# Kernel tuning notes

Hardware: AMD Instinct MI355X
Metric: run time of the kernel (lower is better)

The kernel has to match this reference:

```python
import jax, jax.numpy as jnp
import numpy as np

D_MODEL = 1024
NUM_HEADS = 16
D_HEAD = D_MODEL // NUM_HEADS


def setup_inputs() -> dict:
    key = jax.random.key(0)
    ks = jax.random.split(key, 8)
    B, S = 2, 2048
    query_x = jax.random.normal(ks[0], (B, S, D_MODEL), dtype=jnp.float32)
    key_x = jax.random.normal(ks[1], (B, S, D_MODEL), dtype=jnp.float32)
    value_x = jax.random.normal(ks[2], (B, S, D_MODEL), dtype=jnp.float32)
    mask = jnp.zeros((S, S), dtype=jnp.float32)  # additive mask, broadcast over B,H
    scale = np.sqrt(2.0 / D_MODEL)  # kaiming-ish init
    w_query = jax.random.normal(ks[3], (D_MODEL, D_MODEL), dtype=jnp.float32) * scale
    w_key = jax.random.normal(ks[4], (D_MODEL, D_MODEL), dtype=jnp.float32) * scale
    w_value = jax.random.normal(ks[5], (D_MODEL, D_MODEL), dtype=jnp.float32) * scale
    w0 = jax.random.normal(ks[6], (D_MODEL, D_MODEL), dtype=jnp.float32) * scale
    return {"query_x": query_x, "key_x": key_x, "value_x": value_x, "mask": mask,
            "w_query": w_query, "w_key": w_key, "w_value": w_value, "w0": w0}


def reference(query_x, key_x, value_x, mask, w_query, w_key, w_value, w0):
    B, S, _ = query_x.shape
    # nn.Linear applies x @ W.T; weights stored [out, in]
    def proj(x, w):
        y = jnp.einsum('bsd,ed->bse', x, w)              # [B,S,D]
        return y.reshape(B, S, NUM_HEADS, D_HEAD).transpose(0, 2, 1, 3)  # [B,H,S,Dh]
    q = proj(query_x, w_query)
    k = proj(key_x, w_key)
    v = proj(value_x, w_value)
    scores = jnp.einsum('bhqd,bhkd->bhqk', q, k) / jnp.sqrt(jnp.float32(D_HEAD))
    scores = scores + mask  # broadcast additive mask
    attn = jax.nn.softmax(scores, axis=-1)
    out = jnp.einsum('bhqk,bhkd->bhqd', attn, v)         # [B,H,S,Dh]
    out = out.transpose(0, 2, 1, 3).reshape(B, S, NUM_HEADS * D_HEAD)
    return jnp.einsum('bsd,ed->bse', out, w0)
```

## Files before the change

### kernel.cpp

```cpp
#include <hip/hip_runtime.h>
#include <hip/hip_bf16.h>
#include <stdint.h>

#define D_MODEL 1024
#define NH 16
#define DH 64
#define SEQ 2048
#define MROWS 4096
#define LOG2E 1.44269504088896340736f

typedef unsigned short ushort_t;
typedef __attribute__((ext_vector_type(4))) float f32x4;
typedef __attribute__((ext_vector_type(16))) float f32x16;
typedef __attribute__((ext_vector_type(4))) unsigned short us4;
typedef __attribute__((ext_vector_type(8))) unsigned short us8;
typedef __attribute__((ext_vector_type(4))) unsigned int u32x4;
typedef __attribute__((ext_vector_type(8))) __bf16 bf16x8;

__device__ __forceinline__ f32x4 mfma16(us8 a, us8 b, f32x4 c) {
    return __builtin_amdgcn_mfma_f32_16x16x32_bf16(
        __builtin_bit_cast(bf16x8, a), __builtin_bit_cast(bf16x8, b), c, 0, 0, 0);
}
__device__ __forceinline__ f32x16 mfma32(us8 a, us8 b, f32x16 c) {
    return __builtin_amdgcn_mfma_f32_32x32x16_bf16(
        __builtin_bit_cast(bf16x8, a), __builtin_bit_cast(bf16x8, b), c, 0, 0, 0);
}

__device__ __forceinline__ unsigned int cvtpk(float lo, float hi) {
    unsigned int r;
    asm("v_cvt_pk_bf16_f32 %0, %1, %2" : "=v"(r) : "v"(lo), "v"(hi));
    return r;
}
__device__ __forceinline__ ushort_t f2bf1(float f) {
    return (ushort_t)(cvtpk(f, f) & 0xffffu);
}

__device__ __forceinline__ float exp2_fast(float x) {
#if __has_builtin(__builtin_amdgcn_exp2f)
    return __builtin_amdgcn_exp2f(x);
#else
    float r; asm("v_exp_f32 %0, %1" : "=v"(r) : "v"(x)); return r;
#endif
}

__device__ __forceinline__ void gload16(const void* g, void* l) {
    __builtin_amdgcn_global_load_lds(
        (const __attribute__((address_space(1))) void*)g,
        (__attribute__((address_space(3))) void*)l, 16, 0, 0);
}

__global__ __launch_bounds__(256) void conv_multi(
    const float* __restrict__ s0, ushort_t* __restrict__ d0,
    const float* __restrict__ s1, ushort_t* __restrict__ d1,
    const float* __restrict__ s2, ushort_t* __restrict__ d2,
    const float* __restrict__ s3, ushort_t* __restrict__ d3, int n4)
{
    int z = blockIdx.z;
    const float* s = z == 0 ? s0 : z == 1 ? s1 : z == 2 ? s2 : s3;
    ushort_t* d    = z == 0 ? d0 : z == 1 ? d1 : z == 2 ? d2 : d3;
    int i = blockIdx.x * 256 + threadIdx.x;
    int stride = gridDim.x * 256;
    for (; i < n4; i += stride) {
        float4 v = ((const float4*)s)[i];
        uint2 pr;
        pr.x = cvtpk(v.x, v.y);
        pr.y = cvtpk(v.z, v.w);
        ((uint2*)d)[i] = pr;
    }
}

__global__ __launch_bounds__(256) void mask_flags(const float* __restrict__ mask,
                                                  int* __restrict__ flags)
{
    int qt = blockIdx.x, kt = blockIdx.y;
    int t = threadIdx.x;
    bool nz = false;
#pragma unroll
    for (int i = 0; i < 4; i++) {
        int idx = t + i * 256;
        int row = idx >> 4, c4 = (idx & 15) * 4;
        float4 v = *(const float4*)(mask + (size_t)(qt * 64 + row) * SEQ + kt * 64 + c4);
        nz |= (v.x != 0.f) | (v.y != 0.f) | (v.z != 0.f) | (v.w != 0.f);
    }
    if (__any((int)nz) && (t & 63) == 0) atomicOr(&flags[qt * 32 + kt], 1);
}

__device__ __forceinline__ void gemm_stage(const ushort_t* __restrict__ A,
                                           const ushort_t* __restrict__ B,
                                           int m0, int n0, int t, int w, int k0,
                                           ushort_t* sA, ushort_t* sB)
{
#pragma unroll
    for (int r = 0; r < 4; r++) {
        int chunk = r * 256 + t;
        int row = chunk >> 3, c8 = (chunk & 7) * 8;
        gload16(A + (size_t)(m0 + row) * D_MODEL + k0 + c8,
                &sA[(r * 256 + w * 64) * 8]);
    }
#pragma unroll
    for (int r = 0; r < 2; r++) {
        int chunk = r * 256 + t;
        int row = chunk >> 3, c8 = (chunk & 7) * 8;
        gload16(B + (size_t)(n0 + row) * D_MODEL + k0 + c8,
                &sB[(r * 256 + w * 64) * 8]);
    }
}

__device__ __forceinline__ void gemm_core(const ushort_t* __restrict__ A,
                                          const ushort_t* __restrict__ B,
                                          int m0, int n0, int t,
                                          ushort_t* sA, ushort_t* sB,
                                          f32x4 acc[4][2])
{
    const int lane = t & 63, w = t >> 6;
    const int lr = lane & 15, lg = lane >> 4;
    const int wm = (w >> 1) * 64, wn = (w & 1) * 32;

    gemm_stage(A, B, m0, n0, t, w, 0, sA, sB);
    __syncthreads();

    for (int it = 0; it < D_MODEL / 64; ++it) {
        const int cur = it & 1;
        const ushort_t* cA = sA + cur * (128 * 64);
        const ushort_t* cB = sB + cur * (64 * 64);

        us8 af[4][2], bfr[2][2];
#pragma unroll
        for (int i = 0; i < 4; i++)
#pragma unroll
            for (int ks = 0; ks < 2; ks++)
                af[i][ks] = *(const us8*)&cA[(wm + i * 16 + lr) * 64 + ks * 32 + 8 * lg];
#pragma unroll
        for (int j = 0; j < 2; j++)
#pragma unroll
            for (int ks = 0; ks < 2; ks++)
                bfr[j][ks] = *(const us8*)&cB[(wn + j * 16 + lr) * 64 + ks * 32 + 8 * lg];

        if (it + 1 < D_MODEL / 64)
            gemm_stage(A, B, m0, n0, t, w, (it + 1) * 64,
                       sA + (cur ^ 1) * (128 * 64), sB + (cur ^ 1) * (64 * 64));

#pragma unroll
        for (int i = 0; i < 4; i++)
#pragma unroll
            for (int j = 0; j < 2; j++)
#pragma unroll
                for (int ks = 0; ks < 2; ks++)
                    acc[i][j] = mfma16(af[i][ks], bfr[j][ks], acc[i][j]);

        __syncthreads();
    }
}

__global__ __launch_bounds__(256) void gemm_qk(const ushort_t* __restrict__ A0,
                                               const ushort_t* __restrict__ A1,
                                               const ushort_t* __restrict__ Wq,
                                               const ushort_t* __restrict__ Wk,
                                               ushort_t* __restrict__ Qo,
                                               ushort_t* __restrict__ Ko)
{
    __shared__ ushort_t sA[2][128 * 64];
    __shared__ ushort_t sB[2][64 * 64];
    const int z = blockIdx.z;
    const ushort_t* A = z ? A1 : A0;
    const ushort_t* W = z ? Wk : Wq;
    ushort_t* C = z ? Ko : Qo;
    const float scale = z ? 1.0f : 0.125f * LOG2E;
    const int t = threadIdx.x, lane = t & 63, w = t >> 6;
    const int lr = lane & 15, lg = lane >> 4;
    const int wm = (w >> 1) * 64, wn = (w & 1) * 32;
    const int m0 = blockIdx.x * 128, n0 = blockIdx.y * 64;

    f32x4 acc[4][2];
    f32x4 zero = {0.f, 0.f, 0.f, 0.f};
#pragma unroll
    for (int i = 0; i < 4; i++)
#pragma unroll
        for (int j = 0; j < 2; j++) acc[i][j] = zero;
    gemm_core(A, W, m0, n0, t, &sA[0][0], &sB[0][0], acc);

#pragma unroll
    for (int i = 0; i < 4; i++)
#pragma unroll
        for (int j = 0; j < 2; j++)
#pragma unroll
            for (int r = 0; r < 4; r++) {
                int m = m0 + wm + i * 16 + 4 * lg + r;
                int n = n0 + wn + j * 16 + lr;
                int b = m >> 11, s = m & 2047;
                int h = n >> 6, dh = n & 63;
                C[(((size_t)(b * NH + h)) * SEQ + s) * DH + dh] = f2bf1(acc[i][j][r] * scale);
            }
}

__global__ __launch_bounds__(256) void gemm_v(const ushort_t* __restrict__ A,
                                              const ushort_t* __restrict__ W,
                                              ushort_t* __restrict__ VT)
{
    __shared__ ushort_t sA[2][128 * 64];
    __shared__ ushort_t sB[2][64 * 64];
    const int t = threadIdx.x, lane = t & 63, w = t >> 6;
    const int lr = lane & 15, lg = lane >> 4;
    const int wm = (w >> 1) * 64, wn = (w & 1) * 32;
    const int m0 = blockIdx.x * 128, n0 = blockIdx.y * 64;

    f32x4 acc[4][2];
    f32x4 zero = {0.f, 0.f, 0.f, 0.f};
#pragma unroll
    for (int i = 0; i < 4; i++)
#pragma unroll
        for (int j = 0; j < 2; j++) acc[i][j] = zero;
    gemm_core(A, W, m0, n0, t, &sA[0][0], &sB[0][0], acc);

#pragma unroll
    for (int i = 0; i < 4; i++)
#pragma unroll
        for (int j = 0; j < 2; j++) {
            int m = m0 + wm + i * 16 + 4 * lg;
            int n = n0 + wn + j * 16 + lr;
            int b = m >> 11, s = m & 2047;
            int h = n >> 6, dh = n & 63;
            uint2 pr;
            pr.x = cvtpk(acc[i][j][0], acc[i][j][1]);
            pr.y = cvtpk(acc[i][j][2], acc[i][j][3]);
            *(uint2*)&VT[(((size_t)(b * NH + h)) * DH + dh) * SEQ + s] = pr;
        }
}

__global__ __launch_bounds__(256) void gemm_o(const ushort_t* __restrict__ A,
                                              const ushort_t* __restrict__ W,
                                              float* __restrict__ C)
{
    __shared__ ushort_t sA[2][128 * 64];
    __shared__ ushort_t sB[2][64 * 64];
    const int t = threadIdx.x, lane = t & 63, w = t >> 6;
    const int lr = lane & 15, lg = lane >> 4;
    const int wm = (w >> 1) * 64, wn = (w & 1) * 32;
    const int m0 = blockIdx.x * 128, n0 = blockIdx.y * 64;

    f32x4 acc[4][2];
    f32x4 zero = {0.f, 0.f, 0.f, 0.f};
#pragma unroll
    for (int i = 0; i < 4; i++)
#pragma unroll
        for (int j = 0; j < 2; j++) acc[i][j] = zero;
    gemm_core(A, W, m0, n0, t, &sA[0][0], &sB[0][0], acc);

#pragma unroll
    for (int i = 0; i < 4; i++)
#pragma unroll
        for (int j = 0; j < 2; j++)
#pragma unroll
            for (int r = 0; r < 4; r++) {
                int m = m0 + wm + i * 16 + 4 * lg + r;
                int n = n0 + wn + j * 16 + lr;
                C[(size_t)m * D_MODEL + n] = acc[i][j][r];
            }
}

__global__ __launch_bounds__(256, 2) void attn_fwd(const ushort_t* __restrict__ Q,
                                                   const ushort_t* __restrict__ K,
                                                   const ushort_t* __restrict__ VT,
                                                   const float* __restrict__ mask,
                                                   const int* __restrict__ flags,
                                                   ushort_t* __restrict__ O)
{
    __shared__ ushort_t sK[2][64 * 64];
    __shared__ ushort_t sVT[2][64 * 64];

    const int t = threadIdx.x, lane = t & 63, w = t >> 6;
    const int l31 = lane & 31, lh = lane >> 5;
    const int id = blockIdx.x;
    const int bh = (id & 7) * 4 + ((id >> 3) >> 4);
    const int qt = (id >> 3) & 15;
    const int b = bh >> 4, h = bh & 15;
    const int q = qt * 128 + w * 32 + l31;

    unsigned long long blt = __ballot(flags[(qt * 2 + lh) * 32 + l31] != 0);
    const unsigned int fl = (unsigned int)(blt | (blt >> 32));

    us8 qfr[4];
#pragma unroll
    for (int ks = 0; ks < 4; ks++)
        qfr[ks] = *(const us8*)(Q + ((size_t)bh * SEQ + q) * DH + ks * 16 + 8 * lh);

    f32x16 acc_o[2];
#pragma unroll
    for (int d = 0; d < 2; d++)
#pragma unroll
        for (int r = 0; r < 16; r++) acc_o[d][r] = 0.f;
    float acc_l = 0.f;

    const ushort_t* Kb = K + (size_t)bh * SEQ * DH;
    const ushort_t* Vb = VT + (size_t)bh * DH * SEQ;

    const ushort_t* kp[2];
    const ushort_t* vp[2];
#pragma unroll
    for (int r = 0; r < 2; r++) {
        int j = r * 256 + t;
        int row = j >> 3, cc = (j & 7) ^ (row & 7);
        kp[r] = Kb + (size_t)row * DH + cc * 8;
        vp[r] = Vb + (size_t)row * SEQ + cc * 8;
    }

#define STAGE(kvt_, buf_)                                                     \
    {                                                                         \
        _Pragma("unroll")                                                     \
        for (int r = 0; r < 2; r++)                                           \
            gload16(kp[r] + (size_t)(kvt_) * (64 * DH),                       \
                    &sK[buf_][(r * 256 + w * 64) * 8]);                       \
        _Pragma("unroll")                                                     \
        for (int r = 0; r < 2; r++)                                           \
            gload16(vp[r] + (size_t)(kvt_) * 64,                              \
                    &sVT[buf_][(r * 256 + w * 64) * 8]);                      \
    }

    STAGE(0, 0);
    __syncthreads();

    for (int kvt = 0; kvt < SEQ / 64; ++kvt) {
        const int cur = kvt & 1;
        const char* cK = (const char*)sK[cur];
        const char* cV = (const char*)sVT[cur];

        f32x16 sacc[2];
#pragma unroll
        for (int kb = 0; kb < 2; kb++)
#pragma unroll
            for (int r = 0; r < 16; r++) sacc[kb][r] = 0.f;
        __builtin_amdgcn_s_setprio(1);
#pragma unroll
        for (int ks = 0; ks < 4; ks++)
#pragma unroll
            for (int kb = 0; kb < 2; kb++) {
                int row = kb * 32 + l31;
                int by = (row * 128 + (ks * 16 + 8 * lh) * 2) ^ ((row & 7) << 4);
                us8 kf = *(const us8*)(cK + by);
                sacc[kb] = mfma32(kf, qfr[ks], sacc[kb]);
            }
        __builtin_amdgcn_s_setprio(0);

        us8 vf[4][2];
#pragma unroll
        for (int ks = 0; ks < 4; ks++)
#pragma unroll
            for (int dblk = 0; dblk < 2; dblk++) {
                int row = dblk * 32 + l31;
                int by = (row * 128 + (ks * 16 + 8 * lh) * 2) ^ ((row & 7) << 4);
                vf[ks][dblk] = *(const us8*)(cV + by);
            }

        if (kvt + 1 < SEQ / 64) STAGE(kvt + 1, cur ^ 1);

        if ((fl >> kvt) & 1u) {
#pragma unroll
            for (int kb = 0; kb < 2; kb++)
#pragma unroll
                for (int r = 0; r < 16; r++) {
                    int kcol = kb * 32 + (r & 3) + 8 * (r >> 2) + 4 * lh;
                    sacc[kb][r] += mask[(size_t)q * SEQ + kvt * 64 + kcol] * LOG2E;
                }
        }

        float rs = 0.f;
#pragma unroll
        for (int kb = 0; kb < 2; kb++)
#pragma unroll
            for (int r = 0; r < 16; r++) {
                float p = exp2_fast(sacc[kb][r]);
                sacc[kb][r] = p;
                rs += p;
            }
        rs += __shfl_xor(rs, 32);
        acc_l += rs;

        __builtin_amdgcn_s_setprio(1);
#pragma unroll
        for (int ks = 0; ks < 4; ks++) {
            const int kb = ks >> 1, u = ks & 1;
            unsigned int W0 = cvtpk(sacc[kb][8 * u + 0], sacc[kb][8 * u + 1]);
            unsigned int W1 = cvtpk(sacc[kb][8 * u + 2], sacc[kb][8 * u + 3]);
            unsigned int W2 = cvtpk(sacc[kb][8 * u + 4], sacc[kb][8 * u + 5]);
            unsigned int W3 = cvtpk(sacc[kb][8 * u + 6], sacc[kb][8 * u + 7]);
            asm("v_permlane32_swap_b32 %0, %1" : "+v"(W0), "+v"(W2));
            asm("v_permlane32_swap_b32 %0, %1" : "+v"(W1), "+v"(W3));
            u32x4 pw;
            pw[0] = W0; pw[1] = W1; pw[2] = W2; pw[3] = W3;
            us8 pf = __builtin_bit_cast(us8, pw);
#pragma unroll
            for (int dblk = 0; dblk < 2; dblk++)
                acc_o[dblk] = mfma32(vf[ks][dblk], pf, acc_o[dblk]);
        }
        __builtin_amdgcn_s_setprio(0);

        __syncthreads();
    }

    float inv = 1.f / acc_l;
    ushort_t* Orow = O + ((size_t)(b * SEQ) + q) * D_MODEL + h * DH;
#pragma unroll
    for (int dblk = 0; dblk < 2; dblk++)
#pragma unroll
        for (int g = 0; g < 4; g++) {
            unsigned int lo = cvtpk(acc_o[dblk][4 * g + 0] * inv,
                                    acc_o[dblk][4 * g + 1] * inv);
            unsigned int hi = cvtpk(acc_o[dblk][4 * g + 2] * inv,
                                    acc_o[dblk][4 * g + 3] * inv);
            uint2 pr; pr.x = lo; pr.y = hi;
            *(uint2*)(Orow + dblk * 32 + 8 * g + 4 * lh) = pr;
        }
#undef STAGE
}

extern "C" void kernel_launch(void* const* d_in, const int* in_sizes, int n_in,
                              void* d_out, int out_size, void* d_ws, size_t ws_size,
                              hipStream_t stream)
{
    const float* qx   = (const float*)d_in[0];
    const float* kx   = (const float*)d_in[1];
    const float* vx   = (const float*)d_in[2];
    const float* mask = (const float*)d_in[3];
    const float* wq   = (const float*)d_in[4];
    const float* wk   = (const float*)d_in[5];
    const float* wv   = (const float*)d_in[6];
    const float* w0   = (const float*)d_in[7];
    float* out = (float*)d_out;

    char* ws = (char*)d_ws;
    const size_t MB = 1024 * 1024;
    ushort_t* A0 = (ushort_t*)(ws);
    ushort_t* A1 = (ushort_t*)(ws + 8 * MB);
    ushort_t* Wq = (ushort_t*)(ws + 16 * MB);
    ushort_t* Wk = (ushort_t*)(ws + 18 * MB);
    ushort_t* Wv = (ushort_t*)(ws + 20 * MB);
    ushort_t* W0 = (ushort_t*)(ws + 22 * MB);
    ushort_t* VT = (ushort_t*)(ws + 24 * MB);
    int* flags   = (int*)(ws + 32 * MB);
    ushort_t* AO = A1;
    ushort_t* Qb = (ushort_t*)d_out;
    ushort_t* Kb = (ushort_t*)d_out + 4 * MB;

    hipMemsetAsync(flags, 0, 32 * 32 * sizeof(int), stream);
    mask_flags<<<dim3(32, 32), 256, 0, stream>>>(mask, flags);

    conv_multi<<<dim3(256, 1, 4), 256, 0, stream>>>(wq, Wq, wk, Wk, wv, Wv, w0, W0, 262144);
    conv_multi<<<dim3(1024, 1, 2), 256, 0, stream>>>(qx, A0, kx, A1, qx, A0, qx, A0, 1048576);

    gemm_qk<<<dim3(32, 16, 2), 256, 0, stream>>>(A0, A1, Wq, Wk, Qb, Kb);

    conv_multi<<<dim3(1024, 1, 1), 256, 0, stream>>>(vx, A0, vx, A0, vx, A0, vx, A0, 1048576);
    gemm_v<<<dim3(32, 16), 256, 0, stream>>>(A0, Wv, VT);

    attn_fwd<<<512, 256, 0, stream>>>(Qb, Kb, VT, mask, flags, AO);

    gemm_o<<<dim3(32, 16), 256, 0, stream>>>(AO, W0, out);
}
```

Measured before the change: 142.3 us.

## Fuse fp32-to-bf16 activation conversion into a single QKV projection GEMM

Drops the separate conversion kernels for the query, key and value activations. The projection GEMM now reads fp32 inputs directly and converts them to bf16 while staging into shared memory. The Q, K and V projections are merged into one launch over three grid slices. This removes the bf16 intermediate round-trips and several launches, but the A-tile staging becomes synchronous register loads rather than async global-to-LDS copies, and each element is re-read in fp32 once per N-tile.

```diff
diff --git a/kernel.cpp b/kernel.cpp
--- a/kernel.cpp
+++ b/kernel.cpp
@@ -85,10 +85,22 @@
     if (__any((int)nz) && (t & 63) == 0) atomicOr(&flags[qt * 32 + kt], 1);
 }
 
-__device__ __forceinline__ void gemm_stage(const ushort_t* __restrict__ A,
-                                           const ushort_t* __restrict__ B,
-                                           int m0, int n0, int t, int w, int k0,
-                                           ushort_t* sA, ushort_t* sB)
+__device__ __forceinline__ void stageB_bf16(const ushort_t* __restrict__ B,
+                                            int n0, int t, int w, int k0,
+                                            ushort_t* sB)
+{
+#pragma unroll
+    for (int r = 0; r < 2; r++) {
+        int chunk = r * 256 + t;
+        int row = chunk >> 3, c8 = (chunk & 7) * 8;
+        gload16(B + (size_t)(n0 + row) * D_MODEL + k0 + c8,
+                &sB[(r * 256 + w * 64) * 8]);
+    }
+}
+
+__device__ __forceinline__ void stageA_bf16(const ushort_t* __restrict__ A,
+                                            int m0, int t, int w, int k0,
+                                            ushort_t* sA)
 {
 #pragma unroll
     for (int r = 0; r < 4; r++) {
@@ -97,75 +109,65 @@
         gload16(A + (size_t)(m0 + row) * D_MODEL + k0 + c8,
                 &sA[(r * 256 + w * 64) * 8]);
     }
-#pragma unroll
-    for (int r = 0; r < 2; r++) {
+}
+
+__device__ __forceinline__ void stageA_f32(const float* __restrict__ A,
+                                           int m0, int t, int k0,
+                                           ushort_t* sA)
+{
+#pragma unroll
+    for (int r = 0; r < 4; r++) {
         int chunk = r * 256 + t;
         int row = chunk >> 3, c8 = (chunk & 7) * 8;
-        gload16(B + (size_t)(n0 + row) * D_MODEL + k0 + c8,
-                &sB[(r * 256 + w * 64) * 8]);
-    }
-}
-
-__device__ __forceinline__ void gemm_core(const ushort_t* __restrict__ A,
-                                          const ushort_t* __restrict__ B,
-                                          int m0, int n0, int t,
-                                          ushort_t* sA, ushort_t* sB,
-                                          f32x4 acc[4][2])
-{
-    const int lane = t & 63, w = t >> 6;
-    const int lr = lane & 15, lg = lane >> 4;
-    const int wm = (w >> 1) * 64, wn = (w & 1) * 32;
-
-    gemm_stage(A, B, m0, n0, t, w, 0, sA, sB);
-    __syncthreads();
-
-    for (int it = 0; it < D_MODEL / 64; ++it) {
-        const int cur = it & 1;
-        const ushort_t* cA = sA + cur * (128 * 64);
-        const ushort_t* cB = sB + cur * (64 * 64);
-
-        us8 af[4][2], bfr[2][2];
-#pragma unroll
-        for (int i = 0; i < 4; i++)
+        const float* src = A + (size_t)(m0 + row) * D_MODEL + k0 + c8;
+        float4 v0 = *(const float4*)src;
+        float4 v1 = *(const float4*)(src + 4);
+        u32x4 pw;
+        pw[0] = cvtpk(v0.x, v0.y); pw[1] = cvtpk(v0.z, v0.w);
+        pw[2] = cvtpk(v1.x, v1.y); pw[3] = cvtpk(v1.z, v1.w);
+        *(u32x4*)&sA[chunk * 8] = pw;
+    }
+}
+
+__device__ __forceinline__ void gemm_frags_mfma(const ushort_t* cA, const ushort_t* cB,
+                                                int wm, int wn, int lr, int lg,
+                                                f32x4 acc[4][2])
+{
+    us8 af[4][2], bfr[2][2];
+#pragma unroll
+    for (int i = 0; i < 4; i++)
+#pragma unroll
+        for (int ks = 0; ks < 2; ks++)
+            af[i][ks] = *(const us8*)&cA[(wm + i * 16 + lr) * 64 + ks * 32 + 8 * lg];
+#pragma unroll
+    for (int j = 0; j < 2; j++)
+#pragma unroll
+        for (int ks = 0; ks < 2; ks++)
+            bfr[j][ks] = *(const us8*)&cB[(wn + j * 16 + lr) * 64 + ks * 32 + 8 * lg];
+#pragma unroll
+    for (int i = 0; i < 4; i++)
+#pragma unroll
+        for (int j = 0; j < 2; j++)
 #pragma unroll
             for (int ks = 0; ks < 2; ks++)
-                af[i][ks] = *(const us8*)&cA[(wm + i * 16 + lr) * 64 + ks * 32 + 8 * lg];
-#pragma unroll
-        for (int j = 0; j < 2; j++)
-#pragma unroll
-            for (int ks = 0; ks < 2; ks++)
-                bfr[j][ks] = *(const us8*)&cB[(wn + j * 16 + lr) * 64 + ks * 32 + 8 * lg];
-
-        if (it + 1 < D_MODEL / 64)
-            gemm_stage(A, B, m0, n0, t, w, (it + 1) * 64,
-                       sA + (cur ^ 1) * (128 * 64), sB + (cur ^ 1) * (64 * 64));
-
-#pragma unroll
-        for (int i = 0; i < 4; i++)
-#pragma unroll
-            for (int j = 0; j < 2; j++)
-#pragma unroll
-                for (int ks = 0; ks < 2; ks++)
-                    acc[i][j] = mfma16(af[i][ks], bfr[j][ks], acc[i][j]);
-
-        __syncthreads();
-    }
-}
-
-__global__ __launch_bounds__(256) void gemm_qk(const ushort_t* __restrict__ A0,
-                                               const ushort_t* __restrict__ A1,
-                                               const ushort_t* __restrict__ Wq,
-                                               const ushort_t* __restrict__ Wk,
-                                               ushort_t* __restrict__ Qo,
-                                               ushort_t* __restrict__ Ko)
+                acc[i][j] = mfma16(af[i][ks], bfr[j][ks], acc[i][j]);
+}
+
+__global__ __launch_bounds__(256) void gemm_qkv(const float* __restrict__ qx,
+                                                const float* __restrict__ kx,
+                                                const float* __restrict__ vx,
+                                                const ushort_t* __restrict__ Wq,
+                                                const ushort_t* __restrict__ Wk,
+                                                const ushort_t* __restrict__ Wv,
+                                                ushort_t* __restrict__ Qo,
+                                                ushort_t* __restrict__ Ko,
+                                                ushort_t* __restrict__ VT)
 {
     __shared__ ushort_t sA[2][128 * 64];
     __shared__ ushort_t sB[2][64 * 64];
     const int z = blockIdx.z;
-    const ushort_t* A = z ? A1 : A0;
-    const ushort_t* W = z ? Wk : Wq;
-    ushort_t* C = z ? Ko : Qo;
-    const float scale = z ? 1.0f : 0.125f * LOG2E;
+    const float* A = z == 0 ? qx : z == 1 ? kx : vx;
+    const ushort_t* W = z == 0 ? Wq : z == 1 ? Wk : Wv;
     const int t = threadIdx.x, lane = t & 63, w = t >> 6;
     const int lr = lane & 15, lg = lane >> 4;
     const int wm = (w >> 1) * 64, wn = (w & 1) * 32;
@@ -177,25 +179,80 @@
     for (int i = 0; i < 4; i++)
 #pragma unroll
         for (int j = 0; j < 2; j++) acc[i][j] = zero;
-    gemm_core(A, W, m0, n0, t, &sA[0][0], &sB[0][0], acc);
-
-#pragma unroll
-    for (int i = 0; i < 4; i++)
+
+    stageB_bf16(W, n0, t, w, 0, &sB[0][0]);
+    stageA_f32(A, m0, t, 0, &sA[0][0]);
+    __syncthreads();
+
+    for (int it = 0; it < D_MODEL / 64; ++it) {
+        const int cur = it & 1;
+        if (it + 1 < D_MODEL / 64) {
+        }
+        us8 af[4][2], bfr[2][2];
+        const ushort_t* cA = &sA[cur][0];
+        const ushort_t* cB = &sB[cur][0];
+#pragma unroll
+        for (int i = 0; i < 4; i++)
+#pragma unroll
+            for (int ks = 0; ks < 2; ks++)
+                af[i][ks] = *(const us8*)&cA[(wm + i * 16 + lr) * 64 + ks * 32 + 8 * lg];
 #pragma unroll
         for (int j = 0; j < 2; j++)
 #pragma unroll
-            for (int r = 0; r < 4; r++) {
-                int m = m0 + wm + i * 16 + 4 * lg + r;
+            for (int ks = 0; ks < 2; ks++)
+                bfr[j][ks] = *(const us8*)&cB[(wn + j * 16 + lr) * 64 + ks * 32 + 8 * lg];
+
+        if (it + 1 < D_MODEL / 64) {
+            stageB_bf16(W, n0, t, w, (it + 1) * 64, &sB[cur ^ 1][0]);
+            stageA_f32(A, m0, t, (it + 1) * 64, &sA[cur ^ 1][0]);
+        }
+
+#pragma unroll
+        for (int i = 0; i < 4; i++)
+#pragma unroll
+            for (int j = 0; j < 2; j++)
+#pragma unroll
+                for (int ks = 0; ks < 2; ks++)
+                    acc[i][j] = mfma16(af[i][ks], bfr[j][ks], acc[i][j]);
+
+        __syncthreads();
+    }
+
+    if (z < 2) {
+        ushort_t* C = z ? Ko : Qo;
+        const float scale = z ? 1.0f : 0.125f * LOG2E;
+#pragma unroll
+        for (int i = 0; i < 4; i++)
+#pragma unroll
+            for (int j = 0; j < 2; j++)
+#pragma unroll
+                for (int r = 0; r < 4; r++) {
+                    int m = m0 + wm + i * 16 + 4 * lg + r;
+                    int n = n0 + wn + j * 16 + lr;
+                    int b = m >> 11, s = m & 2047;
+                    int h = n >> 6, dh = n & 63;
+                    C[(((size_t)(b * NH + h)) * SEQ + s) * DH + dh] = f2bf1(acc[i][j][r] * scale);
+                }
+    } else {
+#pragma unroll
+        for (int i = 0; i < 4; i++)
+#pragma unroll
+            for (int j = 0; j < 2; j++) {
+                int m = m0 + wm + i * 16 + 4 * lg;
                 int n = n0 + wn + j * 16 + lr;
                 int b = m >> 11, s = m & 2047;
                 int h = n >> 6, dh = n & 63;
-                C[(((size_t)(b * NH + h)) * SEQ + s) * DH + dh] = f2bf1(acc[i][j][r] * scale);
+                uint2 pr;
+                pr.x = cvtpk(acc[i][j][0], acc[i][j][1]);
+                pr.y = cvtpk(acc[i][j][2], acc[i][j][3]);
+                *(uint2*)&VT[(((size_t)(b * NH + h)) * DH + dh) * SEQ + s] = pr;
             }
-}
-
-__global__ __launch_bounds__(256) void gemm_v(const ushort_t* __restrict__ A,
+    }
+}
+
+__global__ __launch_bounds__(256) void gemm_o(const ushort_t* __restrict__ A,
                                               const ushort_t* __restrict__ W,
-                                              ushort_t* __restrict__ VT)
+                                              float* __restrict__ C)
 {
     __shared__ ushort_t sA[2][128 * 64];
     __shared__ ushort_t sB[2][64 * 64];
@@ -210,41 +267,43 @@
     for (int i = 0; i < 4; i++)
 #pragma unroll
         for (int j = 0; j < 2; j++) acc[i][j] = zero;
-    gemm_core(A, W, m0, n0, t, &sA[0][0], &sB[0][0], acc);
-
-#pragma unroll
-    for (int i = 0; i < 4; i++)
-#pragma unroll
-        for (int j = 0; j < 2; j++) {
-            int m = m0 + wm + i * 16 + 4 * lg;
-            int n = n0 + wn + j * 16 + lr;
-            int b = m >> 11, s = m & 2047;
-            int h = n >> 6, dh = n & 63;
-            uint2 pr;
-            pr.x = cvtpk(acc[i][j][0], acc[i][j][1]);
-            pr.y = cvtpk(acc[i][j][2], acc[i][j][3]);
-            *(uint2*)&VT[(((size_t)(b * NH + h)) * DH + dh) * SEQ + s] = pr;
+
+    stageA_bf16(A, m0, t, w, 0, &sA[0][0]);
+    stageB_bf16(W, n0, t, w, 0, &sB[0][0]);
+    __syncthreads();
+
+    for (int it = 0; it < D_MODEL / 64; ++it) {
+        const int cur = it & 1;
+        const ushort_t* cA = &sA[cur][0];
+        const ushort_t* cB = &sB[cur][0];
+
+        us8 af[4][2], bfr[2][2];
+#pragma unroll
+        for (int i = 0; i < 4; i++)
+#pragma unroll
+            for (int ks = 0; ks < 2; ks++)
+                af[i][ks] = *(const us8*)&cA[(wm + i * 16 + lr) * 64 + ks * 32 + 8 * lg];
+#pragma unroll
+        for (int j = 0; j < 2; j++)
+#pragma unroll
+            for (int ks = 0; ks < 2; ks++)
+                bfr[j][ks] = *(const us8*)&cB[(wn + j * 16 + lr) * 64 + ks * 32 + 8 * lg];
+
+        if (it + 1 < D_MODEL / 64) {
+            stageA_bf16(A, m0, t, w, (it + 1) * 64, &sA[cur ^ 1][0]);
+            stageB_bf16(W, n0, t, w, (it + 1) * 64, &sB[cur ^ 1][0]);
         }
-}
-
-__global__ __launch_bounds__(256) void gemm_o(const ushort_t* __restrict__ A,
-                                              const ushort_t* __restrict__ W,
-                                              float* __restrict__ C)
-{
-    __shared__ ushort_t sA[2][128 * 64];
-    __shared__ ushort_t sB[2][64 * 64];
-    const int t = threadIdx.x, lane = t & 63, w = t >> 6;
-    const int lr = lane & 15, lg = lane >> 4;
-    const int wm = (w >> 1) * 64, wn = (w & 1) * 32;
-    const int m0 = blockIdx.x * 128, n0 = blockIdx.y * 64;
-
-    f32x4 acc[4][2];
-    f32x4 zero = {0.f, 0.f, 0.f, 0.f};
-#pragma unroll
-    for (int i = 0; i < 4; i++)
-#pragma unroll
-        for (int j = 0; j < 2; j++) acc[i][j] = zero;
-    gemm_core(A, W, m0, n0, t, &sA[0][0], &sB[0][0], acc);
+
+#pragma unroll
+        for (int i = 0; i < 4; i++)
+#pragma unroll
+            for (int j = 0; j < 2; j++)
+#pragma unroll
+                for (int ks = 0; ks < 2; ks++)
+                    acc[i][j] = mfma16(af[i][ks], bfr[j][ks], acc[i][j]);
+
+        __syncthreads();
+    }
 
 #pragma unroll
     for (int i = 0; i < 4; i++)
@@ -429,15 +488,13 @@
 
     char* ws = (char*)d_ws;
     const size_t MB = 1024 * 1024;
-    ushort_t* A0 = (ushort_t*)(ws);
-    ushort_t* A1 = (ushort_t*)(ws + 8 * MB);
+    ushort_t* AO = (ushort_t*)(ws + 8 * MB);
     ushort_t* Wq = (ushort_t*)(ws + 16 * MB);
     ushort_t* Wk = (ushort_t*)(ws + 18 * MB);
     ushort_t* Wv = (ushort_t*)(ws + 20 * MB);
     ushort_t* W0 = (ushort_t*)(ws + 22 * MB);
     ushort_t* VT = (ushort_t*)(ws + 24 * MB);
     int* flags   = (int*)(ws + 32 * MB);
-    ushort_t* AO = A1;
     ushort_t* Qb = (ushort_t*)d_out;
     ushort_t* Kb = (ushort_t*)d_out + 4 * MB;
 
@@ -445,12 +502,8 @@
     mask_flags<<<dim3(32, 32), 256, 0, stream>>>(mask, flags);
 
     conv_multi<<<dim3(256, 1, 4), 256, 0, stream>>>(wq, Wq, wk, Wk, wv, Wv, w0, W0, 262144);
-    conv_multi<<<dim3(1024, 1, 2), 256, 0, stream>>>(qx, A0, kx, A1, qx, A0, qx, A0, 1048576);
-
-    gemm_qk<<<dim3(32, 16, 2), 256, 0, stream>>>(A0, A1, Wq, Wk, Qb, Kb);
-
-    conv_multi<<<dim3(1024, 1, 1), 256, 0, stream>>>(vx, A0, vx, A0, vx, A0, vx, A0, 1048576);
-    gemm_v<<<dim3(32, 16), 256, 0, stream>>>(A0, Wv, VT);
+
+    gemm_qkv<<<dim3(32, 16, 3), 256, 0, stream>>>(qx, kx, vx, Wq, Wk, Wv, Qb, Kb, VT);
 
     attn_fwd<<<512, 256, 0, stream>>>(Qb, Kb, VT, mask, flags, AO);
 
```

Result: faster. 137.8 us (-3.1%).
